# Kernel tuning notes

Measured on AMD Instinct MI355X. Metric: run time of the kernel, lower is better.

The kernel has to match this reference:

```python
import jax, jax.numpy as jnp
import numpy as np

D_MODEL = 2048
N_HEADS = 16
D_K = D_MODEL // N_HEADS
B = 2
S = 2048


def setup_inputs() -> dict:
    key = jax.random.key(0)
    ks = jax.random.split(key, 6)
    scale = 1.0 / np.sqrt(D_MODEL)
    return {
        "inp": jax.random.normal(ks[0], (B, S, D_MODEL), dtype=jnp.float32),
        "wq": jax.random.normal(ks[1], (D_MODEL, D_MODEL), dtype=jnp.float32) * scale,
        "wk": jax.random.normal(ks[2], (D_MODEL, D_MODEL), dtype=jnp.float32) * scale,
        "wv": jax.random.normal(ks[3], (D_MODEL, D_MODEL), dtype=jnp.float32) * scale,
        "wo": jax.random.normal(ks[4], (D_MODEL, D_MODEL), dtype=jnp.float32) * scale,
        "attn_bias": jax.random.normal(ks[5], (1, 1, S, S), dtype=jnp.float32),
        "softcap": 30,
    }


def reference(inp, wq, wk, wv, wo, attn_bias, softcap):
    # inp: [B, S, D]; weights stored torch-style [out, in] -> x @ W^T
    b, s, _ = inp.shape

    def split_heads(x):  # [B,S,D] -> [B,H,S,dk]
        return x.reshape(b, s, N_HEADS, D_K).transpose(0, 2, 1, 3)

    q = split_heads(inp @ wq.T)
    k = split_heads(inp @ wk.T)
    v = split_heads(inp @ wv.T)

    scale = 1.0 / np.sqrt(D_K).astype(np.float32)
    scores = jnp.einsum("bhqd,bhkd->bhqk", q, k) * scale + attn_bias
    cap = jnp.float32(softcap)
    scores = jnp.tanh(scores / cap) * cap  # softcap > 0 branch
    weights = jax.nn.softmax(scores, axis=-1)
    o = jnp.einsum("bhqk,bhkd->bhqd", weights, v)
    o = o.transpose(0, 2, 1, 3).reshape(b, s, D_MODEL)
    return o @ wo.T
```

## Files before the change

### kernel.cpp

```cpp
#include <hip/hip_runtime.h>

#define D_MODEL 2048
#define S_LEN 2048
#define NB 2
#define NH 16
#define DK 128

typedef __attribute__((ext_vector_type(8))) __bf16 bf16x8;
typedef __attribute__((ext_vector_type(4))) float f32x4;
typedef __attribute__((ext_vector_type(2))) float f32x2;

__device__ __forceinline__ unsigned short f2bf(float f) {
    union { __bf16 b; unsigned short u; } cv;
    cv.b = (__bf16)f;
    return cv.u;
}

__device__ __forceinline__ f32x2 pk_fma(f32x2 a, f32x2 b, f32x2 c) {
    f32x2 d;
    asm("v_pk_fma_f32 %0, %1, %2, %3" : "=v"(d) : "v"(a), "v"(b), "v"(c));
    return d;
}
__device__ __forceinline__ f32x2 pk_mul(f32x2 a, f32x2 b) {
    f32x2 d;
    asm("v_pk_mul_f32 %0, %1, %2" : "=v"(d) : "v"(a), "v"(b));
    return d;
}

__device__ __forceinline__ void gld_lds16(const void* g, void* l) {
    __builtin_amdgcn_global_load_lds(
        (const __attribute__((address_space(1))) unsigned int*)g,
        (__attribute__((address_space(3))) unsigned int*)l, 16, 0, 0);
}

__global__ void cast_all_f32_to_bf16(const float* __restrict__ x0, const float* __restrict__ x1,
                                     const float* __restrict__ x2, const float* __restrict__ x3,
                                     const float* __restrict__ x4,
                                     unsigned short* y0, unsigned short* y1,
                                     unsigned short* y2, unsigned short* y3,
                                     unsigned short* y4, int n0, int nw) {
    const int sel = blockIdx.y;
    const float* x = (sel == 0) ? x0 : (sel == 1) ? x1 : (sel == 2) ? x2 : (sel == 3) ? x3 : x4;
    unsigned short* y = (sel == 0) ? y0 : (sel == 1) ? y1 : (sel == 2) ? y2 : (sel == 3) ? y3 : y4;
    const int n4 = (sel == 0) ? n0 : nw;
    int i = blockIdx.x * blockDim.x + threadIdx.x;
    int stride = gridDim.x * blockDim.x;
    const float4* x4p = (const float4*)x;
    ushort4* y4p = (ushort4*)y;
    for (; i < n4; i += stride) {
        float4 v = x4p[i];
        ushort4 o;
        o.x = f2bf(v.x); o.y = f2bf(v.y); o.z = f2bf(v.z); o.w = f2bf(v.w);
        y4p[i] = o;
    }
}

#define BM 128
#define BN 128
#define BK 64

__device__ __forceinline__ void cstore(float* p, float v) { *p = v; }
__device__ __forceinline__ void cstore(unsigned short* p, float v) { *p = f2bf(v); }

template <typename OutT>
__device__ __forceinline__ void gemm_body(const unsigned short* __restrict__ A,
                                          const unsigned short* __restrict__ Bt,
                                          OutT* __restrict__ C,
                                          int M, int N, int K, int m0, int n0) {
    __shared__ __align__(16) unsigned short As[BM * BK];
    __shared__ __align__(16) unsigned short Bs[BN * BK];
    const int tid = threadIdx.x;
    const int lane = tid & 63;
    const int wave = tid >> 6;
    const int quad = lane >> 4;
    const int l15 = lane & 15;
    const int wr = (wave >> 1) * 64;
    const int wc = (wave & 1) * 64;

    const int slotbase = wave * 64 + lane;

    f32x4 zero = {0.f, 0.f, 0.f, 0.f};
    f32x4 acc[4][4];
    for (int i = 0; i < 4; i++)
        for (int j = 0; j < 4; j++) acc[i][j] = zero;

    for (int k0 = 0; k0 < K; k0 += BK) {
        __syncthreads();
#pragma unroll
        for (int t = 0; t < 4; t++) {
            int slot = t * 256 + slotbase;
            int row = slot >> 3;
            int cg = (slot & 7) ^ (row & 7);
            gld_lds16(A + (size_t)(m0 + row) * K + k0 + cg * 8, &As[slot * 8]);
            gld_lds16(Bt + (size_t)(n0 + row) * K + k0 + cg * 8, &Bs[slot * 8]);
        }
        __syncthreads();

        bf16x8 af[4][2], bfr[4][2];
#pragma unroll
        for (int t = 0; t < 4; t++)
#pragma unroll
            for (int c = 0; c < 2; c++) {
                int ch = (c * 4 + quad) ^ (l15 & 7);
                af[t][c]  = *(const bf16x8*)(&As[((wr + t * 16 + l15) * 8 + ch) * 8]);
                bfr[t][c] = *(const bf16x8*)(&Bs[((wc + t * 16 + l15) * 8 + ch) * 8]);
            }
#pragma unroll
        for (int c = 0; c < 2; c++)
#pragma unroll
            for (int mt = 0; mt < 4; mt++)
#pragma unroll
                for (int nt = 0; nt < 4; nt++)
                    acc[mt][nt] = __builtin_amdgcn_mfma_f32_16x16x32_bf16(
                        af[mt][c], bfr[nt][c], acc[mt][nt], 0, 0, 0);
    }

#pragma unroll
    for (int mt = 0; mt < 4; mt++)
#pragma unroll
        for (int nt = 0; nt < 4; nt++)
#pragma unroll
            for (int r = 0; r < 4; r++) {
                int m = m0 + wr + mt * 16 + quad * 4 + r;
                int n = n0 + wc + nt * 16 + l15;
                cstore(&C[(size_t)m * N + n], acc[mt][nt][r]);
            }
}

template <typename OutT>
__global__ __launch_bounds__(256) void gemm_bt(const unsigned short* __restrict__ A,
                                               const unsigned short* __restrict__ Bt,
                                               OutT* __restrict__ C,
                                               int M, int N, int K) {
    gemm_body(A, Bt, C, M, N, K, blockIdx.x * BM, blockIdx.y * BN);
}

__global__ __launch_bounds__(256) void gemm_qkv(const unsigned short* __restrict__ X,
                                                const unsigned short* __restrict__ Wq,
                                                const unsigned short* __restrict__ Wk,
                                                const unsigned short* __restrict__ Wv,
                                                unsigned short* __restrict__ Qo,
                                                unsigned short* __restrict__ Ko,
                                                unsigned short* __restrict__ Vto) {
    const int y = blockIdx.y;
    const unsigned short *A, *Bt;
    unsigned short* C;
    int M, N, m0, n0;
    if (y < 32) {
        const int sel = y >> 4;
        A = X;
        Bt = sel ? Wk : Wq;
        C = sel ? Ko : Qo;
        M = NB * S_LEN; N = D_MODEL;
        m0 = blockIdx.x * BM;
        n0 = (y & 15) * BN;
    } else {
        A = Wv; Bt = X; C = Vto;
        M = D_MODEL; N = NB * S_LEN;
        m0 = (y - 32) * BM;
        n0 = blockIdx.x * BN;
    }
    gemm_body(A, Bt, C, M, N, D_MODEL, m0, n0);
}

#define QT 128
#define PS_STRIDE 72
#define NT (S_LEN / 64)

__global__ __launch_bounds__(512, 4) void flash_attn(
        const unsigned short* __restrict__ Q,
        const unsigned short* __restrict__ K,
        const unsigned short* __restrict__ Vt,
        const float* __restrict__ bias,
        const int* __restrict__ softcap,
        unsigned short* __restrict__ O) {
    __shared__ __align__(16) unsigned short Ks[64 * DK];
    __shared__ __align__(16) unsigned short Vts[2][DK * 64];
    __shared__ __align__(16) unsigned short Ps[8 * 16 * PS_STRIDE];

    const int tid = threadIdx.x;
    const int lane = tid & 63;
    const int wave = tid >> 6;
    const int quad = lane >> 4;
    const int l15 = lane & 15;
    const int q0 = blockIdx.x * QT;
    const int h = blockIdx.y;
    const int b = blockIdx.z;

    const float scale = 0.08838834764831845f;
    const float cap = (float)softcap[0];
    const float LOG2E = 1.4426950408889634f;
    const float kz1 = scale / cap;
    const float kz2 = 1.0f / cap;
    const float KK = cap * LOG2E;

    const f32x2 kz1v = {kz1, kz1};
    const f32x2 kz2v = {kz2, kz2};
    const f32x2 KKv  = {KK, KK};
    const f32x2 mKKv = {-KK, -KK};
    const f32x2 c7v  = {-0.05396825397f, -0.05396825397f};
    const f32x2 c5v  = {0.13333333333f, 0.13333333333f};
    const f32x2 c3v  = {-0.33333333333f, -0.33333333333f};
    const f32x2 onev = {1.0f, 1.0f};

    const size_t head_off = (size_t)b * S_LEN * D_MODEL + (size_t)h * DK;
    const size_t vt_row = (size_t)NB * S_LEN;
    const unsigned short* Vh = Vt + (size_t)h * DK * vt_row + (size_t)b * S_LEN;

    bf16x8 qf[4];
    {
        const unsigned short* Qp = Q + head_off + (size_t)(q0 + wave * 16 + l15) * D_MODEL;
#pragma unroll
        for (int c = 0; c < 4; c++)
            qf[c] = *(const bf16x8*)(Qp + c * 32 + quad * 8);
    }

    f32x4 zero = {0.f, 0.f, 0.f, 0.f};
    float l_part[4] = {0.f, 0.f, 0.f, 0.f};
    f32x4 o_acc[8];
#pragma unroll
    for (int d = 0; d < 8; d++) o_acc[d] = zero;

    unsigned short* Psw = &Ps[wave * 16 * PS_STRIDE];
    const int qrow = q0 + wave * 16 + quad * 4;

    auto stageK = [&](int kbase) {
#pragma unroll
        for (int t = 0; t < 2; t++) {
            int slot = t * 512 + tid;
            int kr = slot >> 4;
            int kc = (slot & 15) ^ (kr & 15);
            gld_lds16(K + head_off + (size_t)(kbase + kr) * D_MODEL + kc * 8,
                      &Ks[slot * 8]);
        }
    };
    auto stageV = [&](int kbase, int buf) {
#pragma unroll
        for (int t = 0; t < 2; t++) {
            int slot = t * 512 + tid;
            int vr = slot >> 3;
            int vc = (slot & 7) ^ (vr & 7);
            gld_lds16(Vh + (size_t)vr * vt_row + kbase + vc * 8,
                      &Vts[buf][slot * 8]);
        }
    };

    stageK(0);
    stageV(0, 0);

    for (int kt = 0; kt < NT; kt++) {
        const int kbase = kt * 64;
        __syncthreads();

        f32x4 s[4];
#pragma unroll
        for (int nt = 0; nt < 4; nt++) s[nt] = zero;
        __builtin_amdgcn_s_setprio(1);
#pragma unroll
        for (int c = 0; c < 4; c++) {
            bf16x8 kf[4];
#pragma unroll
            for (int nt = 0; nt < 4; nt++)
                kf[nt] = *(const bf16x8*)(&Ks[((nt * 16 + l15) * 16 +
                                               ((c * 4 + quad) ^ l15)) * 8]);
#pragma unroll
            for (int nt = 0; nt < 4; nt++)
                s[nt] = __builtin_amdgcn_mfma_f32_16x16x32_bf16(qf[c], kf[nt], s[nt], 0, 0, 0);
        }
        __builtin_amdgcn_s_setprio(0);

        __syncthreads();

        f32x2 bb2[4][2];
#pragma unroll
        for (int nt = 0; nt < 4; nt++) {
            const float* bp = bias + (size_t)qrow * S_LEN + kbase + nt * 16 + l15;
            f32x2 lo, hi;
            lo.x = bp[0];
            lo.y = bp[(size_t)S_LEN];
            hi.x = bp[(size_t)2 * S_LEN];
            hi.y = bp[(size_t)3 * S_LEN];
            bb2[nt][0] = lo;
            bb2[nt][1] = hi;
        }
        __builtin_amdgcn_sched_barrier(0);

        if (kt + 1 < NT) {
            stageK(kbase + 64);
            stageV(kbase + 64, (kt + 1) & 1);
        }

#pragma unroll
        for (int nt = 0; nt < 4; nt++) {
            {
                f32x2 sv = __builtin_shufflevector(s[nt], s[nt], 0, 1);
                f32x2 z = pk_fma(sv, kz1v, pk_mul(bb2[nt][0], kz2v));
                f32x2 z2 = pk_mul(z, z);
                f32x2 w = pk_fma(z2, c7v, c5v);
                w = pk_fma(z2, w, c3v);
                w = pk_fma(z2, w, onev);
                f32x2 t = pk_mul(z, w);
                f32x2 arg = pk_fma(t, KKv, mKKv);
                float p0 = __builtin_amdgcn_exp2f(arg.x);
                float p1 = __builtin_amdgcn_exp2f(arg.y);
                s[nt][0] = p0; s[nt][1] = p1;
                l_part[0] += p0; l_part[1] += p1;
            }
            {
                f32x2 sv = __builtin_shufflevector(s[nt], s[nt], 2, 3);
                f32x2 z = pk_fma(sv, kz1v, pk_mul(bb2[nt][1], kz2v));
                f32x2 z2 = pk_mul(z, z);
                f32x2 w = pk_fma(z2, c7v, c5v);
                w = pk_fma(z2, w, c3v);
                w = pk_fma(z2, w, onev);
                f32x2 t = pk_mul(z, w);
                f32x2 arg = pk_fma(t, KKv, mKKv);
                float p2 = __builtin_amdgcn_exp2f(arg.x);
                float p3 = __builtin_amdgcn_exp2f(arg.y);
                s[nt][2] = p2; s[nt][3] = p3;
                l_part[2] += p2; l_part[3] += p3;
            }
        }

#pragma unroll
        for (int nt = 0; nt < 4; nt++)
#pragma unroll
            for (int r = 0; r < 4; r++)
                Psw[(quad * 4 + r) * PS_STRIDE + nt * 16 + l15] = f2bf(s[nt][r]);

        const unsigned short* Vcur = Vts[kt & 1];
        __builtin_amdgcn_s_setprio(1);
#pragma unroll
        for (int c = 0; c < 2; c++) {
            bf16x8 pf = *(const bf16x8*)(&Psw[l15 * PS_STRIDE + c * 32 + quad * 8]);
#pragma unroll
            for (int dt = 0; dt < 8; dt++) {
                bf16x8 vf = *(const bf16x8*)(&Vcur[((dt * 16 + l15) * 8 +
                                                    ((c * 4 + quad) ^ (l15 & 7))) * 8]);
                o_acc[dt] = __builtin_amdgcn_mfma_f32_16x16x32_bf16(pf, vf, o_acc[dt], 0, 0, 0);
            }
        }
        __builtin_amdgcn_s_setprio(0);
    }

#pragma unroll
    for (int r = 0; r < 4; r++) {
        float l = l_part[r];
        l += __shfl_xor(l, 1, 64);
        l += __shfl_xor(l, 2, 64);
        l += __shfl_xor(l, 4, 64);
        l += __shfl_xor(l, 8, 64);
        float inv = 1.0f / l;
        int row = qrow + r;
        unsigned short* Op = O + (size_t)(b * S_LEN + row) * D_MODEL + h * DK;
#pragma unroll
        for (int dt = 0; dt < 8; dt++)
            Op[dt * 16 + l15] = f2bf(o_acc[dt][r] * inv);
    }
}

extern "C" void kernel_launch(void* const* d_in, const int* in_sizes, int n_in,
                              void* d_out, int out_size, void* d_ws, size_t ws_size,
                              hipStream_t stream) {
    const float* inp = (const float*)d_in[0];
    const float* wq  = (const float*)d_in[1];
    const float* wk  = (const float*)d_in[2];
    const float* wv  = (const float*)d_in[3];
    const float* wo  = (const float*)d_in[4];
    const float* bias = (const float*)d_in[5];
    const int* softcap = (const int*)d_in[6];
    float* out = (float*)d_out;

    unsigned short* ws = (unsigned short*)d_ws;
    const size_t n_inp = (size_t)NB * S_LEN * D_MODEL;
    const size_t n_w = (size_t)D_MODEL * D_MODEL;
    unsigned short* inp_b = ws;
    unsigned short* wq_b = inp_b + n_inp;
    unsigned short* wk_b = wq_b + n_w;
    unsigned short* wv_b = wk_b + n_w;
    unsigned short* wo_b = wv_b + n_w;
    unsigned short* Qb = wo_b + n_w;
    unsigned short* Kb = Qb + n_inp;
    unsigned short* Vtb = Kb + n_inp;
    unsigned short* Ob = Vtb + n_inp;

    cast_all_f32_to_bf16<<<dim3(512, 5), dim3(256), 0, stream>>>(
        inp, wq, wk, wv, wo, inp_b, wq_b, wk_b, wv_b, wo_b,
        (int)(n_inp / 4), (int)(n_w / 4));

    gemm_qkv<<<dim3(NB * S_LEN / BM, 48), 256, 0, stream>>>(
        inp_b, wq_b, wk_b, wv_b, Qb, Kb, Vtb);

    flash_attn<<<dim3(S_LEN / QT, NH, NB), 512, 0, stream>>>(Qb, Kb, Vtb, bias, softcap, Ob);

    dim3 gg(NB * S_LEN / BM, D_MODEL / BN);
    gemm_bt<float><<<gg, 256, 0, stream>>>(Ob, wo_b, out, NB * S_LEN, D_MODEL, D_MODEL);
}
```

Measured before the change: 412.9 us.

## Rewrite projection GEMMs as 256x256 double-buffered 8-wave pipelined kernels

Replaces the 128x128 single-buffered GEMM with a 256x256 tile run by 512 threads (8 waves). It double-buffers LDS, splits each K-step into four MFMA quadrants, and issues the next tile's global-to-LDS loads between them, raising wave priority around the MFMA blocks. Block IDs are remapped with an XCD-aware swizzle so neighbouring tiles share L2. The larger tiles improve operand reuse and hide load latency, but they use 128KB of LDS and many more accumulator registers. The output GEMM also drops to 128 blocks, which may underfill the 256 CUs.

Result: no change. 419.2 us (+1.5%).

```diff
diff --git a/kernel.cpp b/kernel.cpp
--- a/kernel.cpp
+++ b/kernel.cpp
@@ -55,112 +55,202 @@
     }
 }
 
-#define BM 128
-#define BN 128
-#define BK 64
-
 __device__ __forceinline__ void cstore(float* p, float v) { *p = v; }
 __device__ __forceinline__ void cstore(unsigned short* p, float v) { *p = f2bf(v); }
 
 template <typename OutT>
-__device__ __forceinline__ void gemm_body(const unsigned short* __restrict__ A,
-                                          const unsigned short* __restrict__ Bt,
-                                          OutT* __restrict__ C,
-                                          int M, int N, int K, int m0, int n0) {
-    __shared__ __align__(16) unsigned short As[BM * BK];
-    __shared__ __align__(16) unsigned short Bs[BN * BK];
+__device__ __forceinline__ void gemm8_body(const unsigned short* __restrict__ A,
+                                           const unsigned short* __restrict__ Bt,
+                                           OutT* __restrict__ C,
+                                           int N, int K, int m0, int n0) {
+    __shared__ __align__(16) unsigned short lds[2][32768];
     const int tid = threadIdx.x;
     const int lane = tid & 63;
     const int wave = tid >> 6;
     const int quad = lane >> 4;
     const int l15 = lane & 15;
-    const int wr = (wave >> 1) * 64;
-    const int wc = (wave & 1) * 64;
-
-    const int slotbase = wave * 64 + lane;
+    const int wm = wave >> 2;
+    const int wn = wave & 3;
+    const int swz7 = l15 & 7;
 
     f32x4 zero = {0.f, 0.f, 0.f, 0.f};
-    f32x4 acc[4][4];
-    for (int i = 0; i < 4; i++)
+    f32x4 acc[8][4];
+#pragma unroll
+    for (int i = 0; i < 8; i++)
+#pragma unroll
         for (int j = 0; j < 4; j++) acc[i][j] = zero;
 
-    for (int k0 = 0; k0 < K; k0 += BK) {
-        __syncthreads();
-#pragma unroll
-        for (int t = 0; t < 4; t++) {
-            int slot = t * 256 + slotbase;
-            int row = slot >> 3;
-            int cg = (slot & 7) ^ (row & 7);
-            gld_lds16(A + (size_t)(m0 + row) * K + k0 + cg * 8, &As[slot * 8]);
-            gld_lds16(Bt + (size_t)(n0 + row) * K + k0 + cg * 8, &Bs[slot * 8]);
-        }
-        __syncthreads();
-
-        bf16x8 af[4][2], bfr[4][2];
-#pragma unroll
-        for (int t = 0; t < 4; t++)
-#pragma unroll
-            for (int c = 0; c < 2; c++) {
-                int ch = (c * 4 + quad) ^ (l15 & 7);
-                af[t][c]  = *(const bf16x8*)(&As[((wr + t * 16 + l15) * 8 + ch) * 8]);
-                bfr[t][c] = *(const bf16x8*)(&Bs[((wc + t * 16 + l15) * 8 + ch) * 8]);
-            }
-#pragma unroll
-        for (int c = 0; c < 2; c++)
+    auto stage = [&](int d, int kof, int jlo, int jhi) {
+#pragma unroll
+        for (int j = jlo; j < jhi; ++j) {
+            int lin = j * 512 + tid;
+            int s2 = lin & 2047;
+            int row = s2 >> 3;
+            int cg = (s2 & 7) ^ (row & 7);
+            const unsigned short* src = (j < 4)
+                ? A  + (size_t)(m0 + row) * K + kof + cg * 8
+                : Bt + (size_t)(n0 + row) * K + kof + cg * 8;
+            gld_lds16(src, &lds[d][(j < 4 ? 0 : 16384) + s2 * 8]);
+        }
+    };
+
+    stage(0, 0, 0, 8);
+    asm volatile("s_waitcnt vmcnt(0)" ::: "memory");
+    __builtin_amdgcn_sched_barrier(0);
+    __builtin_amdgcn_s_barrier();
+
+    const int NKT = K >> 6;
+    for (int t = 0; t < NKT; ++t) {
+        const int c = t & 1;
+        const unsigned short* Ab = &lds[c][0];
+        const unsigned short* Bb = &lds[c][16384];
+        const bool pf = (t + 1 < NKT);
+        const int d = c ^ 1;
+        const int kof = (t + 1) << 6;
+
+        bf16x8 a03[4][2], b01[2][2], b23[2][2], a47[4][2];
+
+#pragma unroll
+        for (int mt = 0; mt < 4; mt++)
+#pragma unroll
+            for (int cc = 0; cc < 2; cc++) {
+                int row = wm * 128 + mt * 16 + l15;
+                a03[mt][cc] = *(const bf16x8*)(&Ab[(row * 8 + ((cc * 4 + quad) ^ swz7)) * 8]);
+            }
+#pragma unroll
+        for (int nt = 0; nt < 2; nt++)
+#pragma unroll
+            for (int cc = 0; cc < 2; cc++) {
+                int row = wn * 64 + nt * 16 + l15;
+                b01[nt][cc] = *(const bf16x8*)(&Bb[(row * 8 + ((cc * 4 + quad) ^ swz7)) * 8]);
+            }
+        if (pf) stage(d, kof, 0, 4);
+        __builtin_amdgcn_s_barrier();
+        asm volatile("s_waitcnt lgkmcnt(0)" ::: "memory");
+        __builtin_amdgcn_sched_barrier(0);
+        __builtin_amdgcn_s_setprio(1);
+#pragma unroll
+        for (int cc = 0; cc < 2; cc++)
 #pragma unroll
             for (int mt = 0; mt < 4; mt++)
 #pragma unroll
-                for (int nt = 0; nt < 4; nt++)
+                for (int nt = 0; nt < 2; nt++)
                     acc[mt][nt] = __builtin_amdgcn_mfma_f32_16x16x32_bf16(
-                        af[mt][c], bfr[nt][c], acc[mt][nt], 0, 0, 0);
-    }
-
-#pragma unroll
-    for (int mt = 0; mt < 4; mt++)
+                        a03[mt][cc], b01[nt][cc], acc[mt][nt], 0, 0, 0);
+        __builtin_amdgcn_s_setprio(0);
+        __builtin_amdgcn_s_barrier();
+
+#pragma unroll
+        for (int nt = 0; nt < 2; nt++)
+#pragma unroll
+            for (int cc = 0; cc < 2; cc++) {
+                int row = wn * 64 + (nt + 2) * 16 + l15;
+                b23[nt][cc] = *(const bf16x8*)(&Bb[(row * 8 + ((cc * 4 + quad) ^ swz7)) * 8]);
+            }
+        if (pf) stage(d, kof, 4, 8);
+        __builtin_amdgcn_s_barrier();
+        asm volatile("s_waitcnt lgkmcnt(0)" ::: "memory");
+        __builtin_amdgcn_sched_barrier(0);
+        __builtin_amdgcn_s_setprio(1);
+#pragma unroll
+        for (int cc = 0; cc < 2; cc++)
+#pragma unroll
+            for (int mt = 0; mt < 4; mt++)
+#pragma unroll
+                for (int nt = 0; nt < 2; nt++)
+                    acc[mt][nt + 2] = __builtin_amdgcn_mfma_f32_16x16x32_bf16(
+                        a03[mt][cc], b23[nt][cc], acc[mt][nt + 2], 0, 0, 0);
+        __builtin_amdgcn_s_setprio(0);
+        __builtin_amdgcn_s_barrier();
+
+#pragma unroll
+        for (int mt = 0; mt < 4; mt++)
+#pragma unroll
+            for (int cc = 0; cc < 2; cc++) {
+                int row = wm * 128 + (mt + 4) * 16 + l15;
+                a47[mt][cc] = *(const bf16x8*)(&Ab[(row * 8 + ((cc * 4 + quad) ^ swz7)) * 8]);
+            }
+        __builtin_amdgcn_s_barrier();
+        asm volatile("s_waitcnt lgkmcnt(0)" ::: "memory");
+        __builtin_amdgcn_sched_barrier(0);
+        __builtin_amdgcn_s_setprio(1);
+#pragma unroll
+        for (int cc = 0; cc < 2; cc++)
+#pragma unroll
+            for (int mt = 0; mt < 4; mt++)
+#pragma unroll
+                for (int nt = 0; nt < 2; nt++)
+                    acc[mt + 4][nt] = __builtin_amdgcn_mfma_f32_16x16x32_bf16(
+                        a47[mt][cc], b01[nt][cc], acc[mt + 4][nt], 0, 0, 0);
+        __builtin_amdgcn_s_setprio(0);
+        __builtin_amdgcn_s_barrier();
+
+        __builtin_amdgcn_s_setprio(1);
+#pragma unroll
+        for (int cc = 0; cc < 2; cc++)
+#pragma unroll
+            for (int mt = 0; mt < 4; mt++)
+#pragma unroll
+                for (int nt = 0; nt < 2; nt++)
+                    acc[mt + 4][nt + 2] = __builtin_amdgcn_mfma_f32_16x16x32_bf16(
+                        a47[mt][cc], b23[nt][cc], acc[mt + 4][nt + 2], 0, 0, 0);
+        __builtin_amdgcn_s_setprio(0);
+        if (pf) {
+            asm volatile("s_waitcnt vmcnt(0)" ::: "memory");
+            __builtin_amdgcn_sched_barrier(0);
+        }
+        __builtin_amdgcn_s_barrier();
+    }
+
+#pragma unroll
+    for (int mt = 0; mt < 8; mt++)
 #pragma unroll
         for (int nt = 0; nt < 4; nt++)
 #pragma unroll
             for (int r = 0; r < 4; r++) {
-                int m = m0 + wr + mt * 16 + quad * 4 + r;
-                int n = n0 + wc + nt * 16 + l15;
+                int m = m0 + wm * 128 + mt * 16 + quad * 4 + r;
+                int n = n0 + wn * 64 + nt * 16 + l15;
                 cstore(&C[(size_t)m * N + n], acc[mt][nt][r]);
             }
 }
 
-template <typename OutT>
-__global__ __launch_bounds__(256) void gemm_bt(const unsigned short* __restrict__ A,
-                                               const unsigned short* __restrict__ Bt,
-                                               OutT* __restrict__ C,
-                                               int M, int N, int K) {
-    gemm_body(A, Bt, C, M, N, K, blockIdx.x * BM, blockIdx.y * BN);
-}
-
-__global__ __launch_bounds__(256) void gemm_qkv(const unsigned short* __restrict__ X,
-                                                const unsigned short* __restrict__ Wq,
-                                                const unsigned short* __restrict__ Wk,
-                                                const unsigned short* __restrict__ Wv,
-                                                unsigned short* __restrict__ Qo,
-                                                unsigned short* __restrict__ Ko,
-                                                unsigned short* __restrict__ Vto) {
-    const int y = blockIdx.y;
+__global__ __launch_bounds__(512, 2) void gemm8_qkv(const unsigned short* __restrict__ X,
+                                                    const unsigned short* __restrict__ Wq,
+                                                    const unsigned short* __restrict__ Wk,
+                                                    const unsigned short* __restrict__ Wv,
+                                                    unsigned short* __restrict__ Qo,
+                                                    unsigned short* __restrict__ Ko,
+                                                    unsigned short* __restrict__ Vto) {
+    const int bid = blockIdx.x;
+    const int swz = (bid & 7) * 48 + (bid >> 3);
     const unsigned short *A, *Bt;
     unsigned short* C;
-    int M, N, m0, n0;
-    if (y < 32) {
-        const int sel = y >> 4;
-        A = X;
-        Bt = sel ? Wk : Wq;
-        C = sel ? Ko : Qo;
-        M = NB * S_LEN; N = D_MODEL;
-        m0 = blockIdx.x * BM;
-        n0 = (y & 15) * BN;
+    int N, m0, n0;
+    if (swz < 256) {
+        const int sel = swz >> 7;
+        const int id = swz & 127;
+        A = X; Bt = sel ? Wk : Wq; C = sel ? Ko : Qo;
+        N = D_MODEL;
+        m0 = (id >> 3) * 256;
+        n0 = (id & 7) * 256;
     } else {
+        const int id = swz - 256;
         A = Wv; Bt = X; C = Vto;
-        M = D_MODEL; N = NB * S_LEN;
-        m0 = (y - 32) * BM;
-        n0 = blockIdx.x * BN;
-    }
-    gemm_body(A, Bt, C, M, N, D_MODEL, m0, n0);
+        N = NB * S_LEN;
+        m0 = (id >> 4) * 256;
+        n0 = (id & 15) * 256;
+    }
+    gemm8_body<unsigned short>(A, Bt, C, N, D_MODEL, m0, n0);
+}
+
+__global__ __launch_bounds__(512, 2) void gemm8_out(const unsigned short* __restrict__ A,
+                                                    const unsigned short* __restrict__ Bt,
+                                                    float* __restrict__ C) {
+    const int bid = blockIdx.x;
+    const int swz = (bid & 7) * 16 + (bid >> 3);
+    const int m0 = (swz >> 3) * 256;
+    const int n0 = (swz & 7) * 256;
+    gemm8_body<float>(A, Bt, C, D_MODEL, D_MODEL, m0, n0);
 }
 
 #define QT 128
@@ -388,11 +478,9 @@
         inp, wq, wk, wv, wo, inp_b, wq_b, wk_b, wv_b, wo_b,
         (int)(n_inp / 4), (int)(n_w / 4));
 
-    gemm_qkv<<<dim3(NB * S_LEN / BM, 48), 256, 0, stream>>>(
-        inp_b, wq_b, wk_b, wv_b, Qb, Kb, Vtb);
+    gemm8_qkv<<<dim3(384), 512, 0, stream>>>(inp_b, wq_b, wk_b, wv_b, Qb, Kb, Vtb);
 
     flash_attn<<<dim3(S_LEN / QT, NH, NB), 512, 0, stream>>>(Qb, Kb, Vtb, bias, softcap, Ob);
 
-    dim3 gg(NB * S_LEN / BM, D_MODEL / BN);
-    gemm_bt<float><<<gg, 256, 0, stream>>>(Ob, wo_b, out, NB * S_LEN, D_MODEL, D_MODEL);
-}
+    gemm8_out<<<dim3(128), 512, 0, stream>>>(Ob, wo_b, out);
+}
```
